# Optimization experiments

Hardware: AMD Instinct MI355X
Metric: run time of the kernel (lower is better)

Reference implementation:

```python
import jax, jax.numpy as jnp
import numpy as np

N_HEAD = 16

def setup_inputs() -> dict:
    key = jax.random.key(0)
    ks = jax.random.split(key, 4)
    C = 2048
    x = jax.random.normal(ks[0], (4, 2048, C), dtype=jnp.float32)
    # weights stored [in, out] (transpose of torch Linear's [out, in]); same math y = x @ W + b
    w_qkv = jax.random.normal(ks[1], (C, 3 * C), dtype=jnp.float32) * (1.0 / np.sqrt(C))
    b_qkv = jnp.zeros((3 * C,), dtype=jnp.float32)
    w_proj = jax.random.normal(ks[2], (C, C), dtype=jnp.float32) * (1.0 / np.sqrt(C))
    b_proj = jnp.zeros((C,), dtype=jnp.float32)
    return {"x": x, "w_qkv": w_qkv, "b_qkv": b_qkv, "w_proj": w_proj, "b_proj": b_proj}

def reference(x, w_qkv, b_qkv, w_proj, b_proj):
    B, S, C = x.shape
    H = N_HEAD
    D = C // H
    qkv = x @ w_qkv + b_qkv                      # [B,S,3C]
    q, k, v = jnp.split(qkv, 3, axis=-1)
    # [B,H,S,D]
    q = q.reshape(B, S, H, D).transpose(0, 2, 1, 3)
    k = k.reshape(B, S, H, D).transpose(0, 2, 1, 3)
    v = v.reshape(B, S, H, D).transpose(0, 2, 1, 3)
    scale = 1.0 / np.sqrt(D).astype(np.float32)
    scores = jnp.einsum('bhqd,bhkd->bhqk', q, k) * scale   # [B,H,S,S]
    causal = jnp.tril(jnp.ones((S, S), dtype=bool))
    scores = jnp.where(causal, scores, jnp.finfo(scores.dtype).min)
    attn = jax.nn.softmax(scores, axis=-1)
    y = jnp.einsum('bhqk,bhkd->bhqd', attn, v)              # [B,H,S,D]
    y = y.transpose(0, 2, 1, 3).reshape(B, S, C)
    return y @ w_proj + b_proj
```

## Files before the change

kernel.cpp:

```cpp
#include <hip/hip_runtime.h>
#include <hip/hip_bf16.h>

typedef __bf16 bf16x8 __attribute__((ext_vector_type(8)));
typedef float floatx4 __attribute__((ext_vector_type(4)));

__device__ __forceinline__ unsigned short f2bf(float f) {
  unsigned u = __float_as_uint(f);
  u += 0x7fffu + ((u >> 16) & 1u);
  return (unsigned short)(u >> 16);
}

__device__ __forceinline__ unsigned cvt_pk_bf16(float lo, float hi) {
  unsigned r;
  asm("v_cvt_pk_bf16_f32 %0, %1, %2" : "=v"(r) : "v"(lo), "v"(hi));
  return r;
}

__device__ __forceinline__ void async_copy16(const void* g, void* l) {
  __builtin_amdgcn_global_load_lds(
      (const __attribute__((address_space(1))) void*)g,
      (__attribute__((address_space(3))) void*)l, 16, 0, 0);
}

__global__ __launch_bounds__(256) void cvt_bf16(
    const float* __restrict__ in, unsigned short* __restrict__ out) {
  size_t i = ((size_t)blockIdx.x * 256 + threadIdx.x) * 8;
  float4 a0 = *(const float4*)&in[i];
  float4 a1 = *(const float4*)&in[i + 4];
  uint4 d;
  d.x = (unsigned)f2bf(a0.x) | ((unsigned)f2bf(a0.y) << 16);
  d.y = (unsigned)f2bf(a0.z) | ((unsigned)f2bf(a0.w) << 16);
  d.z = (unsigned)f2bf(a1.x) | ((unsigned)f2bf(a1.y) << 16);
  d.w = (unsigned)f2bf(a1.z) | ((unsigned)f2bf(a1.w) << 16);
  *(uint4*)(&out[i]) = d;
}

__global__ __launch_bounds__(256) void transpose_cvt(
    const float* __restrict__ in, unsigned short* __restrict__ out,
    int R, int Ccol) {
  __shared__ unsigned short tile[32][33];
  int c0 = blockIdx.x * 32, r0 = blockIdx.y * 32;
  int tx = threadIdx.x & 31, ty = threadIdx.x >> 5;
  #pragma unroll
  for (int i = 0; i < 32; i += 8)
    tile[ty + i][tx] = f2bf(in[(size_t)(r0 + ty + i) * Ccol + c0 + tx]);
  __syncthreads();
  #pragma unroll
  for (int i = 0; i < 32; i += 8)
    out[(size_t)(c0 + ty + i) * R + r0 + tx] = tile[tx][ty + i];
}

__device__ __forceinline__ void stage_rows256(
    const unsigned short* __restrict__ P, int K, int r0, int k0,
    unsigned short* Ls, int lane, int w) {
  const int lrow = lane >> 3;
  const int gch = (lane & 7) ^ lrow;
  #pragma unroll
  for (int u = 0; u < 4; u++) {
    int g = w * 4 + u;
    int row = g * 8 + lrow;
    async_copy16(&P[(size_t)(r0 + row) * K + k0 + gch * 8], &Ls[g * 512]);
  }
}

__device__ __forceinline__ void gemm_bt_256(
    const unsigned short* __restrict__ A, const unsigned short* __restrict__ Bt,
    int K, int m0, int n0,
    unsigned short* AsB, unsigned short* BsB,
    floatx4 acc[8][4]) {
  const int t = threadIdx.x, lane = t & 63, w = t >> 6;
  const int wr = w >> 2, wc = w & 3;
  const int l15 = lane & 15, l4 = lane >> 4;
  const floatx4 zf = {0.f, 0.f, 0.f, 0.f};
  #pragma unroll
  for (int mi = 0; mi < 8; mi++)
    #pragma unroll
    for (int ni = 0; ni < 4; ni++) acc[mi][ni] = zf;

  const int nkt = K >> 6;
  stage_rows256(A, K, m0, 0, AsB, lane, w);
  stage_rows256(Bt, K, n0, 0, BsB, lane, w);

  #pragma unroll 1
  for (int kt = 0; kt < nkt; kt++) {
    const unsigned short* Ab = AsB + (kt & 1) * 16384;
    const unsigned short* Bb = BsB + (kt & 1) * 16384;
    unsigned short* An = AsB + ((kt + 1) & 1) * 16384;
    unsigned short* Bn = BsB + ((kt + 1) & 1) * 16384;
    const bool pf = (kt + 1 < nkt);
    if (pf) {
      stage_rows256(A, K, m0, (kt + 1) * 64, An, lane, w);
      asm volatile("s_waitcnt vmcnt(4)" ::: "memory");
    } else {
      asm volatile("s_waitcnt vmcnt(0)" ::: "memory");
    }
    __builtin_amdgcn_s_barrier();
    #pragma unroll
    for (int kk = 0; kk < 2; kk++) {
      bf16x8 af[8], bfr[4];
      #pragma unroll
      for (int mi = 0; mi < 8; mi++) {
        int row = wr * 128 + mi * 16 + l15;
        af[mi] = *(const bf16x8*)(
            &Ab[row * 64 + (((kk * 4 + l4) ^ (l15 & 7)) << 3)]);
      }
      #pragma unroll
      for (int ni = 0; ni < 4; ni++) {
        int row = wc * 64 + ni * 16 + l15;
        bfr[ni] = *(const bf16x8*)(
            &Bb[row * 64 + (((kk * 4 + l4) ^ (l15 & 7)) << 3)]);
      }
      if (kk == 0 && pf)
        stage_rows256(Bt, K, n0, (kt + 1) * 64, Bn, lane, w);
      __builtin_amdgcn_s_barrier();
      __builtin_amdgcn_s_setprio(1);
      #pragma unroll
      for (int mi = 0; mi < 8; mi++)
        #pragma unroll
        for (int ni = 0; ni < 4; ni++)
          acc[mi][ni] = __builtin_amdgcn_mfma_f32_16x16x32_bf16(
              af[mi], bfr[ni], acc[mi][ni], 0, 0, 0);
      __builtin_amdgcn_s_setprio(0);
      __builtin_amdgcn_s_barrier();
    }
  }
}

__global__ __launch_bounds__(512, 2) void gemm_qkv(
    const unsigned short* __restrict__ X, const unsigned short* __restrict__ WT,
    const float* __restrict__ bias,
    unsigned short* __restrict__ Qo, unsigned short* __restrict__ Ko,
    unsigned short* __restrict__ Vto) {
  __shared__ unsigned short As[2][256 * 64];
  __shared__ unsigned short Bs[2][256 * 64];
  int lg = blockIdx.x;
  int bn = lg % 24, bm = lg / 24;
  int m0 = bm * 256, n0 = bn * 256;
  floatx4 acc[8][4];
  gemm_bt_256(X, WT, 2048, m0, n0, As[0], Bs[0], acc);

  const int t = threadIdx.x, lane = t & 63, w = t >> 6;
  const int wr = w >> 2, wc = w & 3;
  const int l15 = lane & 15, l4 = lane >> 4;
  int which = n0 >> 11;
  int b = m0 >> 11;
  int s0 = m0 & 2047;
  float bv[4];
  #pragma unroll
  for (int ni = 0; ni < 4; ni++)
    bv[ni] = bias[n0 + wc * 64 + ni * 16 + l15];

  if (which < 2) {
    unsigned short* dst = (which == 0) ? Qo : Ko;
    #pragma unroll
    for (int ni = 0; ni < 4; ni++) {
      int cn = (n0 & 2047) + wc * 64 + ni * 16;
      int h = cn >> 7, d = (cn & 127) + l15;
      size_t base = ((size_t)(b * 16 + h)) * 2048;
      #pragma unroll
      for (int mi = 0; mi < 8; mi++) {
        #pragma unroll
        for (int r = 0; r < 4; r++) {
          int srow = s0 + wr * 128 + mi * 16 + l4 * 4 + r;
          dst[(base + srow) * 128 + d] = f2bf(acc[mi][ni][r] + bv[ni]);
        }
      }
    }
  } else {
    #pragma unroll
    for (int ni = 0; ni < 4; ni++) {
      int cn = (n0 & 2047) + wc * 64 + ni * 16;
      int h = cn >> 7, d = (cn & 127) + l15;
      #pragma unroll
      for (int mi = 0; mi < 8; mi++) {
        int sr = s0 + wr * 128 + mi * 16 + l4 * 4;
        ushort4 v;
        v.x = f2bf(acc[mi][ni][0] + bv[ni]);
        v.y = f2bf(acc[mi][ni][1] + bv[ni]);
        v.z = f2bf(acc[mi][ni][2] + bv[ni]);
        v.w = f2bf(acc[mi][ni][3] + bv[ni]);
        *(ushort4*)(&Vto[((size_t)(b * 16 + h) * 128 + d) * 2048 + sr]) = v;
      }
    }
  }
}

__device__ __forceinline__ void attn_stage(
    const unsigned short* __restrict__ Kb, const unsigned short* __restrict__ Vb,
    __bf16* Ksel, __bf16* Vsel, int k0, int lane, int w) {
  const int krow_in = lane >> 4, kch = lane & 15;
  const int vrow_in = lane >> 3, vch = lane & 7;
  #pragma unroll
  for (int u = 0; u < 2; u++) {
    int uk = w * 2 + u;
    int row = uk * 4 + krow_in;
    int sch = kch ^ (row & 7);
    async_copy16(&Kb[(size_t)(k0 + row) * 128 + sch * 8], Ksel + uk * 512);
  }
  #pragma unroll
  for (int u = 0; u < 2; u++) {
    int uv = w * 2 + u;
    int row = uv * 8 + vrow_in;
    int sch = vch ^ vrow_in;
    async_copy16(&Vb[(size_t)row * 2048 + k0 + sch * 8], Vsel + uv * 512);
  }
}

__global__ __launch_bounds__(512, 4) void attn(
    const unsigned short* __restrict__ Qg, const unsigned short* __restrict__ Kg,
    const unsigned short* __restrict__ Vtg, unsigned short* __restrict__ Yg) {
  const int S = 2048, Dh = 128;
  const float c1 = 0.08838834764831845f * 1.4426950408889634f;
  const float NEG_BIG = -3.0e38f;
  __shared__ __bf16 Ks[2][64 * 128];
  __shared__ __bf16 Vs[2][128 * 64];
  __shared__ __bf16 Ps[8][16 * 64];

  int wg = blockIdx.x;
  int lg = (wg & 7) * 64 + (wg >> 3);
  int qtp = lg & 7;
  int bh = lg >> 3;
  const int t = threadIdx.x, lane = t & 63, w = t >> 6;
  const int l15 = lane & 15, l4 = lane >> 4;
  const unsigned short* Qb = Qg + (size_t)bh * S * Dh;
  const unsigned short* Kb = Kg + (size_t)bh * S * Dh;
  const unsigned short* Vb = Vtg + (size_t)bh * Dh * S;
  __bf16* Pw = Ps[w];
  int b = bh >> 4, h = bh & 15;
  const floatx4 zf = {0.f, 0.f, 0.f, 0.f};

  #pragma unroll 1
  for (int half = 0; half < 2; half++) {
    int jq = half ? qtp : (15 - qtp);
    int qb0 = jq * 128;
    int qrow_base = qb0 + w * 16;
    bf16x8 qf[4];
    #pragma unroll
    for (int kk = 0; kk < 4; kk++)
      qf[kk] = *(const bf16x8*)(
          &Qb[(size_t)(qrow_base + l15) * Dh + kk * 32 + l4 * 8]);
    floatx4 accO[8];
    #pragma unroll
    for (int nd = 0; nd < 8; nd++) accO[nd] = zf;
    float mst = NEG_BIG, lst = 0.f;

    int ntiles = 2 * jq + 2;
    int cur = 0;
    attn_stage(Kb, Vb, Ks[0], Vs[0], 0, lane, w);
    __syncthreads();

    #pragma unroll 1
    for (int kt = 0; kt < ntiles; kt++) {
      if (kt + 1 < ntiles)
        attn_stage(Kb, Vb, Ks[cur ^ 1], Vs[cur ^ 1], (kt + 1) * 64, lane, w);

      const __bf16* Kcur = Ks[cur];
      const __bf16* Vcur = Vs[cur];
      floatx4 sc[4];
      #pragma unroll
      for (int ni = 0; ni < 4; ni++) sc[ni] = zf;
      __builtin_amdgcn_s_setprio(1);
      #pragma unroll
      for (int kk = 0; kk < 4; kk++) {
        bf16x8 kf[4];
        #pragma unroll
        for (int ni = 0; ni < 4; ni++) {
          int row = ni * 16 + l15;
          kf[ni] = *(const bf16x8*)(
              &Kcur[row * 128 + (((kk * 4 + l4) ^ (l15 & 7)) << 3)]);
        }
        #pragma unroll
        for (int ni = 0; ni < 4; ni++)
          sc[ni] = __builtin_amdgcn_mfma_f32_16x16x32_bf16(kf[ni], qf[kk], sc[ni], 0, 0, 0);
      }
      __builtin_amdgcn_s_setprio(0);

      if (kt >= 2 * jq) {
        int kb = kt * 64 - qb0 - w * 16 - l15;
        #pragma unroll
        for (int ni = 0; ni < 4; ni++)
          #pragma unroll
          for (int r = 0; r < 4; r++)
            if (kb + ni * 16 + l4 * 4 + r > 0) sc[ni][r] = NEG_BIG;
      }

      float mt = fmaxf(fmaxf(fmaxf(sc[0][0], sc[0][1]), fmaxf(sc[0][2], sc[0][3])),
                       fmaxf(fmaxf(sc[1][0], sc[1][1]), fmaxf(sc[1][2], sc[1][3])));
      mt = fmaxf(mt,
           fmaxf(fmaxf(fmaxf(sc[2][0], sc[2][1]), fmaxf(sc[2][2], sc[2][3])),
                 fmaxf(fmaxf(sc[3][0], sc[3][1]), fmaxf(sc[3][2], sc[3][3]))));
      mt = fmaxf(mt, __shfl_xor(mt, 16, 64));
      mt = fmaxf(mt, __shfl_xor(mt, 32, 64));

      if (!__all(mt <= mst + 8.0f)) {
        float mnew = fmaxf(mst, mt);
        float alpha = exp2f((mst - mnew) * c1);
        mst = mnew;
        lst *= alpha;
        float ar[4];
        #pragma unroll
        for (int r = 0; r < 4; r++)
          ar[r] = __shfl(alpha, l4 * 20 + r, 64);
        #pragma unroll
        for (int nd = 0; nd < 8; nd++)
          #pragma unroll
          for (int r = 0; r < 4; r++) accO[nd][r] *= ar[r];
      }

      float mc = mst * c1;
      float p[4][4];
      float rs = 0.f;
      #pragma unroll
      for (int ni = 0; ni < 4; ni++)
        #pragma unroll
        for (int r = 0; r < 4; r++) {
          p[ni][r] = exp2f(sc[ni][r] * c1 - mc);
          rs += p[ni][r];
        }
      rs += __shfl_xor(rs, 16, 64);
      rs += __shfl_xor(rs, 32, 64);
      lst += rs;

      #pragma unroll
      for (int ni = 0; ni < 4; ni++) {
        uint2 dw;
        dw.x = cvt_pk_bf16(p[ni][0], p[ni][1]);
        dw.y = cvt_pk_bf16(p[ni][2], p[ni][3]);
        int s = ni * 4 + l4;
        *(uint2*)(&Pw[l15 * 64 + (((s >> 1) ^ (l15 & 7)) << 3) + ((s & 1) << 2)]) = dw;
      }

      __builtin_amdgcn_s_setprio(1);
      #pragma unroll
      for (int kk = 0; kk < 2; kk++) {
        bf16x8 pf = *(const bf16x8*)(
            &Pw[l15 * 64 + (((kk * 4 + l4) ^ (l15 & 7)) << 3)]);
        #pragma unroll
        for (int nd = 0; nd < 8; nd++) {
          int row = nd * 16 + l15;
          bf16x8 vf = *(const bf16x8*)(
              &Vcur[row * 64 + (((kk * 4 + l4) ^ (l15 & 7)) << 3)]);
          accO[nd] = __builtin_amdgcn_mfma_f32_16x16x32_bf16(pf, vf, accO[nd], 0, 0, 0);
        }
      }
      __builtin_amdgcn_s_setprio(0);
      __syncthreads();
      cur ^= 1;
    }

    float invl = 1.0f / lst;
    float ivr[4];
    #pragma unroll
    for (int r = 0; r < 4; r++)
      ivr[r] = __shfl(invl, l4 * 20 + r, 64);
    #pragma unroll
    for (int r = 0; r < 4; r++) {
      int srow = qrow_base + l4 * 4 + r;
      size_t rowbase = ((size_t)(b * 2048 + srow)) * 2048 + h * 128;
      #pragma unroll
      for (int nd = 0; nd < 8; nd++)
        Yg[rowbase + nd * 16 + l15] = f2bf(accO[nd][r] * ivr[r]);
    }
  }
}

__global__ __launch_bounds__(512, 2) void gemm_proj(
    const unsigned short* __restrict__ Yin, const unsigned short* __restrict__ WT,
    const float* __restrict__ bias, float* __restrict__ Og) {
  __shared__ unsigned short As[2][256 * 64];
  __shared__ unsigned short Bs[2][256 * 64];
  int lg = blockIdx.x;
  int bn = lg % 8, bm = lg / 8;
  int m0 = bm * 256, n0 = bn * 256;
  floatx4 acc[8][4];
  gemm_bt_256(Yin, WT, 2048, m0, n0, As[0], Bs[0], acc);

  const int t = threadIdx.x, lane = t & 63, w = t >> 6;
  const int wr = w >> 2, wc = w & 3;
  const int l15 = lane & 15, l4 = lane >> 4;
  float bv[4];
  #pragma unroll
  for (int ni = 0; ni < 4; ni++)
    bv[ni] = bias[n0 + wc * 64 + ni * 16 + l15];
  #pragma unroll
  for (int mi = 0; mi < 8; mi++)
    #pragma unroll
    for (int ni = 0; ni < 4; ni++)
      #pragma unroll
      for (int r = 0; r < 4; r++)
        Og[(size_t)(m0 + wr * 128 + mi * 16 + l4 * 4 + r) * 2048 +
           n0 + wc * 64 + ni * 16 + l15] = acc[mi][ni][r] + bv[ni];
}

extern "C" void kernel_launch(void* const* d_in, const int* in_sizes, int n_in,
                              void* d_out, int out_size, void* d_ws, size_t ws_size,
                              hipStream_t stream) {
  const float* x      = (const float*)d_in[0];
  const float* w_qkv  = (const float*)d_in[1];
  const float* b_qkv  = (const float*)d_in[2];
  const float* w_proj = (const float*)d_in[3];
  const float* b_proj = (const float*)d_in[4];
  float* out = (float*)d_out;
  char* ws = (char*)d_ws;

  unsigned short* Q   = (unsigned short*)d_out;
  unsigned short* Kt  = (unsigned short*)((char*)d_out + 33554432);
  unsigned short* Vt  = (unsigned short*)(ws);
  unsigned short* Xbf = (unsigned short*)(ws + 33554432);
  unsigned short* Y   = (unsigned short*)(ws + 33554432);
  unsigned short* WqT = (unsigned short*)(ws + 67108864);
  unsigned short* WpT = (unsigned short*)(ws + 67108864);

  cvt_bf16<<<dim3(8192), 256, 0, stream>>>(x, Xbf);
  transpose_cvt<<<dim3(192, 64), 256, 0, stream>>>(w_qkv, WqT, 2048, 6144);
  gemm_qkv<<<dim3(768), 512, 0, stream>>>(Xbf, WqT, b_qkv, Q, Kt, Vt);
  attn<<<dim3(512), 512, 0, stream>>>(Q, Kt, Vt, Y);
  transpose_cvt<<<dim3(64, 64), 256, 0, stream>>>(w_proj, WpT, 2048, 2048);
  gemm_proj<<<dim3(256), 512, 0, stream>>>(Y, WpT, b_proj, out);
}
```

Measured before the change: 569.0 us.

## Replace QKV GEMM with single-buffered 128x128 tile kernel

The QKV projection moves from the 256x256 double-buffered, setprio-scheduled GEMM (512 threads, 768 blocks) to a simpler 128x128 tile kernel with 256 threads, single-buffered LDS and two syncthreads per k-step, launched as a 48x64 grid. The smaller tiles give more blocks and higher occupancy (launch bounds 256,3). The cost is lower data reuse per tile, which means more global and LDS traffic, and no overlap of loads with MFMA inside a block. The epilogue is adapted to the new warp layout, with one head per block.

```diff
diff --git a/kernel.cpp b/kernel.cpp
--- a/kernel.cpp
+++ b/kernel.cpp
@@ -48,6 +48,114 @@
   #pragma unroll
   for (int i = 0; i < 32; i += 8)
     out[(size_t)(c0 + ty + i) * R + r0 + tx] = tile[tx][ty + i];
+}
+
+__device__ __forceinline__ void gemm_bt_mainloop(
+    const unsigned short* __restrict__ A, const unsigned short* __restrict__ Bt,
+    int K, int m0, int n0,
+    unsigned short* As, unsigned short* Bs, floatx4 acc[4][4]) {
+  const int t = threadIdx.x;
+  const int lane = t & 63, w = t >> 6;
+  const int wm = w >> 1, wn = w & 1;
+  const int l15 = lane & 15, l4 = lane >> 4;
+  const int lrow = lane >> 3, lchunk = lane & 7;
+  const int gch = lchunk ^ lrow;
+  const floatx4 zf = {0.f, 0.f, 0.f, 0.f};
+  #pragma unroll
+  for (int mi = 0; mi < 4; mi++)
+    #pragma unroll
+    for (int ni = 0; ni < 4; ni++) acc[mi][ni] = zf;
+
+  for (int k0 = 0; k0 < K; k0 += 64) {
+    __syncthreads();
+    #pragma unroll
+    for (int i = 0; i < 4; i++) {
+      int ridx = w * 4 + i;
+      int row = ridx * 8 + lrow;
+      async_copy16(&A[(size_t)(m0 + row) * K + k0 + gch * 8], &As[ridx * 512]);
+    }
+    #pragma unroll
+    for (int i = 0; i < 4; i++) {
+      int ridx = w * 4 + i;
+      int row = ridx * 8 + lrow;
+      async_copy16(&Bt[(size_t)(n0 + row) * K + k0 + gch * 8], &Bs[ridx * 512]);
+    }
+    __syncthreads();
+    #pragma unroll
+    for (int kk = 0; kk < 2; kk++) {
+      bf16x8 af[4], bfr[4];
+      #pragma unroll
+      for (int mi = 0; mi < 4; mi++) {
+        int row = wm * 64 + mi * 16 + l15;
+        af[mi] = *(const bf16x8*)(&As[row * 64 + ((kk * 4 + l4) ^ (l15 & 7)) * 8]);
+      }
+      #pragma unroll
+      for (int ni = 0; ni < 4; ni++) {
+        int row = wn * 64 + ni * 16 + l15;
+        bfr[ni] = *(const bf16x8*)(&Bs[row * 64 + ((kk * 4 + l4) ^ (l15 & 7)) * 8]);
+      }
+      #pragma unroll
+      for (int mi = 0; mi < 4; mi++)
+        #pragma unroll
+        for (int ni = 0; ni < 4; ni++)
+          acc[mi][ni] = __builtin_amdgcn_mfma_f32_16x16x32_bf16(
+              af[mi], bfr[ni], acc[mi][ni], 0, 0, 0);
+    }
+  }
+}
+
+__global__ __launch_bounds__(256, 3) void gemm_qkv(
+    const unsigned short* __restrict__ X, const unsigned short* __restrict__ WT,
+    const float* __restrict__ bias,
+    unsigned short* __restrict__ Qo, unsigned short* __restrict__ Ko,
+    unsigned short* __restrict__ Vto) {
+  __shared__ unsigned short As[128 * 64];
+  __shared__ unsigned short Bs[128 * 64];
+  int n0 = blockIdx.x * 128, m0 = blockIdx.y * 128;
+  floatx4 acc[4][4];
+  gemm_bt_mainloop(X, WT, 2048, m0, n0, As, Bs, acc);
+
+  const int t = threadIdx.x, lane = t & 63, w = t >> 6;
+  const int wm = w >> 1, wn = w & 1;
+  const int l15 = lane & 15, l4 = lane >> 4;
+  int which = n0 >> 11;
+  int h = (n0 & 2047) >> 7;
+  int b = m0 >> 11;
+  int s0 = m0 & 2047;
+  float bv[4];
+  #pragma unroll
+  for (int ni = 0; ni < 4; ni++)
+    bv[ni] = bias[n0 + wn * 64 + ni * 16 + l15];
+
+  if (which < 2) {
+    unsigned short* dst = (which == 0) ? Qo : Ko;
+    size_t base = (size_t)(b * 16 + h) * 2048;
+    #pragma unroll
+    for (int mi = 0; mi < 4; mi++)
+      #pragma unroll
+      for (int ni = 0; ni < 4; ni++) {
+        int d = wn * 64 + ni * 16 + l15;
+        #pragma unroll
+        for (int r = 0; r < 4; r++) {
+          int srow = s0 + wm * 64 + mi * 16 + l4 * 4 + r;
+          dst[(base + srow) * 128 + d] = f2bf(acc[mi][ni][r] + bv[ni]);
+        }
+      }
+  } else {
+    #pragma unroll
+    for (int mi = 0; mi < 4; mi++)
+      #pragma unroll
+      for (int ni = 0; ni < 4; ni++) {
+        int d = wn * 64 + ni * 16 + l15;
+        int sr = s0 + wm * 64 + mi * 16 + l4 * 4;
+        ushort4 v;
+        v.x = f2bf(acc[mi][ni][0] + bv[ni]);
+        v.y = f2bf(acc[mi][ni][1] + bv[ni]);
+        v.z = f2bf(acc[mi][ni][2] + bv[ni]);
+        v.w = f2bf(acc[mi][ni][3] + bv[ni]);
+        *(ushort4*)(&Vto[((size_t)(b * 16 + h) * 128 + d) * 2048 + sr]) = v;
+      }
+  }
 }
 
 __device__ __forceinline__ void stage_rows256(
@@ -126,65 +234,6 @@
   }
 }
 
-__global__ __launch_bounds__(512, 2) void gemm_qkv(
-    const unsigned short* __restrict__ X, const unsigned short* __restrict__ WT,
-    const float* __restrict__ bias,
-    unsigned short* __restrict__ Qo, unsigned short* __restrict__ Ko,
-    unsigned short* __restrict__ Vto) {
-  __shared__ unsigned short As[2][256 * 64];
-  __shared__ unsigned short Bs[2][256 * 64];
-  int lg = blockIdx.x;
-  int bn = lg % 24, bm = lg / 24;
-  int m0 = bm * 256, n0 = bn * 256;
-  floatx4 acc[8][4];
-  gemm_bt_256(X, WT, 2048, m0, n0, As[0], Bs[0], acc);
-
-  const int t = threadIdx.x, lane = t & 63, w = t >> 6;
-  const int wr = w >> 2, wc = w & 3;
-  const int l15 = lane & 15, l4 = lane >> 4;
-  int which = n0 >> 11;
-  int b = m0 >> 11;
-  int s0 = m0 & 2047;
-  float bv[4];
-  #pragma unroll
-  for (int ni = 0; ni < 4; ni++)
-    bv[ni] = bias[n0 + wc * 64 + ni * 16 + l15];
-
-  if (which < 2) {
-    unsigned short* dst = (which == 0) ? Qo : Ko;
-    #pragma unroll
-    for (int ni = 0; ni < 4; ni++) {
-      int cn = (n0 & 2047) + wc * 64 + ni * 16;
-      int h = cn >> 7, d = (cn & 127) + l15;
-      size_t base = ((size_t)(b * 16 + h)) * 2048;
-      #pragma unroll
-      for (int mi = 0; mi < 8; mi++) {
-        #pragma unroll
-        for (int r = 0; r < 4; r++) {
-          int srow = s0 + wr * 128 + mi * 16 + l4 * 4 + r;
-          dst[(base + srow) * 128 + d] = f2bf(acc[mi][ni][r] + bv[ni]);
-        }
-      }
-    }
-  } else {
-    #pragma unroll
-    for (int ni = 0; ni < 4; ni++) {
-      int cn = (n0 & 2047) + wc * 64 + ni * 16;
-      int h = cn >> 7, d = (cn & 127) + l15;
-      #pragma unroll
-      for (int mi = 0; mi < 8; mi++) {
-        int sr = s0 + wr * 128 + mi * 16 + l4 * 4;
-        ushort4 v;
-        v.x = f2bf(acc[mi][ni][0] + bv[ni]);
-        v.y = f2bf(acc[mi][ni][1] + bv[ni]);
-        v.z = f2bf(acc[mi][ni][2] + bv[ni]);
-        v.w = f2bf(acc[mi][ni][3] + bv[ni]);
-        *(ushort4*)(&Vto[((size_t)(b * 16 + h) * 128 + d) * 2048 + sr]) = v;
-      }
-    }
-  }
-}
-
 __device__ __forceinline__ void attn_stage(
     const unsigned short* __restrict__ Kb, const unsigned short* __restrict__ Vb,
     __bf16* Ksel, __bf16* Vsel, int k0, int lane, int w) {
@@ -413,7 +462,7 @@
 
   cvt_bf16<<<dim3(8192), 256, 0, stream>>>(x, Xbf);
   transpose_cvt<<<dim3(192, 64), 256, 0, stream>>>(w_qkv, WqT, 2048, 6144);
-  gemm_qkv<<<dim3(768), 512, 0, stream>>>(Xbf, WqT, b_qkv, Q, Kt, Vt);
+  gemm_qkv<<<dim3(48, 64), 256, 0, stream>>>(Xbf, WqT, b_qkv, Q, Kt, Vt);
   attn<<<dim3(512), 512, 0, stream>>>(Q, Kt, Vt, Y);
   transpose_cvt<<<dim3(64, 64), 256, 0, stream>>>(w_proj, WpT, 2048, 2048);
   gemm_proj<<<dim3(256), 512, 0, stream>>>(Y, WpT, b_proj, out);
```

Result: no change. 578.0 us (+1.6%).
